# Optimization experiments

Hardware: AMD Instinct MI355X
Metric: run time of the kernel (lower is better)

The kernel has to match this reference:

```python
import jax, jax.numpy as jnp
import numpy as np

N, E, F_IN, H, C = 50000, 800000, 128, 4, 73
HC = H * C  # 292
NEG_SLOPE_ATT = 0.2   # GATv2 attention leaky relu
NEG_SLOPE_ACT = 0.01  # F.leaky_relu default
BN_EPS = 1e-5


def setup_inputs() -> dict:
    key = jax.random.key(0)
    ks = jax.random.split(key, 20)
    rn = lambda k, shp, s=0.05: (jax.random.normal(k, shp, jnp.float32) * s)
    inp = {
        'x': jax.random.normal(ks[0], (N, F_IN), jnp.float32),
        'edge_index': jax.random.randint(ks[1], (2, E), 0, N, jnp.int64),
        # conv1 (in=F_IN)
        'Wl1': rn(ks[2], (HC, F_IN)), 'bl1': rn(ks[3], (HC,)),
        'Wr1': rn(ks[4], (HC, F_IN)), 'br1': rn(ks[5], (HC,)),
        'att1': rn(ks[6], (H, C)), 'b1': rn(ks[7], (HC,)),
        # conv2 (in=HC)
        'Wl2': rn(ks[8], (HC, HC)), 'bl2': rn(ks[9], (HC,)),
        'Wr2': rn(ks[10], (HC, HC)), 'br2': rn(ks[11], (HC,)),
        'att2': rn(ks[12], (H, C)), 'b2': rn(ks[13], (HC,)),
        # shared BatchNorm1d(HC)
        'gamma': jnp.ones((HC,), jnp.float32), 'beta': jnp.zeros((HC,), jnp.float32),
        # classifier Linear(HC, 2)
        'Wc': rn(ks[14], (2, HC)), 'bc': rn(ks[15], (2,)),
    }
    return inp


def _gatv2(x, src, dst, Wl, bl, Wr, br, att, b):
    # lin_l on source, lin_r on target (PyG GATv2Conv, share_weights=False)
    xl = (x @ Wl.T + bl).reshape(-1, H, C)  # [N,H,C]
    xr = (x @ Wr.T + br).reshape(-1, H, C)
    f = xl[src] + xr[dst]                    # [E,H,C] edge-wise gather
    s = jnp.einsum('ehc,hc->eh', jax.nn.leaky_relu(f, NEG_SLOPE_ATT), att)
    # segment softmax over incoming edges of each destination node
    m = jax.ops.segment_max(s, dst, num_segments=N)
    ex = jnp.exp(s - m[dst])
    den = jax.ops.segment_sum(ex, dst, num_segments=N)
    alpha = ex / (den[dst] + 1e-16)          # [E,H]
    out = jax.ops.segment_sum(alpha[:, :, None] * xl[src], dst, num_segments=N)
    return out.reshape(-1, HC) + b           # concat heads + bias


def _bn(x, gamma, beta):
    mu = jnp.mean(x, axis=0)
    var = jnp.mean((x - mu) ** 2, axis=0)
    return (x - mu) * jax.lax.rsqrt(var + BN_EPS) * gamma + beta


def reference(x, edge_index, Wl1, bl1, Wr1, br1, att1, b1,
              Wl2, bl2, Wr2, br2, att2, b2, gamma, beta, Wc, bc):
    src, dst = edge_index[0], edge_index[1]
    h = _gatv2(x, src, dst, Wl1, bl1, Wr1, br1, att1, b1)
    h = jax.nn.leaky_relu(_bn(h, gamma, beta), NEG_SLOPE_ACT)
    h = _gatv2(h, src, dst, Wl2, bl2, Wr2, br2, att2, b2)
    h = jax.nn.leaky_relu(_bn(h, gamma, beta), NEG_SLOPE_ACT)
    return h @ Wc.T + bc
```

## Files before the change

### kernel.cpp

```cpp
#include <hip/hip_runtime.h>

#define HCDIM 292
#define NHEAD 4
#define CDIM 73
#define SLOTS 5
#define NPERM 320
#define BN_EPS 1e-5f
#define LOG2E 1.44269504f

using u16x8 = __attribute__((ext_vector_type(8))) unsigned short;
using f32x4 = __attribute__((ext_vector_type(4))) float;
using u16x4 = __attribute__((ext_vector_type(4))) unsigned short;
using hf2   = __attribute__((ext_vector_type(2))) _Float16;
using v2h   = __attribute__((ext_vector_type(2))) __fp16;
using v8h   = __attribute__((ext_vector_type(8))) __fp16;

__device__ inline v2h pkrtz(float a, float b) {
  return __builtin_amdgcn_cvt_pkrtz(a, b);
}
__device__ inline float fdot2(hf2 a, hf2 b, float c) {
  return __builtin_amdgcn_fdot2(__builtin_bit_cast(v2h, a),
                                __builtin_bit_cast(v2h, b), c, false);
}
__device__ inline ushort f2h(float f) {
  _Float16 h = (_Float16)f;
  return __builtin_bit_cast(ushort, h);
}
__device__ inline float h2f(ushort v) {
  return (float)__builtin_bit_cast(_Float16, v);
}
__device__ inline hf2 habs2(hf2 a) {
  unsigned u = __builtin_bit_cast(unsigned, a) & 0x7fff7fffu;
  return __builtin_bit_cast(hf2, u);
}

__device__ inline int perm2feat(int p, bool& valid) {
  int h, c;
  if (p < 256) {
    h = p >> 6;
    c = ((p & 3) << 4) | ((p >> 2) & 15);
    valid = true;
  } else {
    int q = p - 256;
    h = q >> 4;
    c = 64 + (q & 15);
    valid = (q & 15) < (CDIM - 64);
  }
  return h * CDIM + c;
}

__global__ void k_wperm(const float* __restrict__ W, const float* __restrict__ b,
                        ushort* __restrict__ Wp, float* __restrict__ pb,
                        int Kin, int Kpad, int kperm) {
  int p = blockIdx.x, t = threadIdx.x;
  bool pv;
  int gn = perm2feat(p, pv);
  int gk = t;
  bool kv = t < Kin;
  if (kperm) { bool v2; gk = perm2feat(t, v2); kv = v2; }
  ushort v = 0;
  if (pv && kv) v = f2h(W[(size_t)gn * Kin + gk]);
  Wp[(size_t)p * Kpad + t] = v;
  if (t == 0) pb[p] = pv ? b[gn] : 0.f;
}

__global__ void k_vecperm(const float* __restrict__ att1, const float* __restrict__ b1,
                          const float* __restrict__ att2, const float* __restrict__ b2,
                          const float* __restrict__ gamma, const float* __restrict__ beta,
                          const float* __restrict__ Wc, float* __restrict__ o) {
  int p = threadIdx.x, w = blockIdx.x;
  bool pv;
  int gn = perm2feat(p, pv);
  const float* src;
  switch (w) {
    case 0: src = att1; break;
    case 1: src = b1; break;
    case 2: src = att2; break;
    case 3: src = b2; break;
    case 4: src = gamma; break;
    case 5: src = beta; break;
    case 6: src = Wc; break;
    default: src = Wc + HCDIM; break;
  }
  o[w * NPERM + p] = pv ? src[gn] : 0.f;
}

__global__ void k_hist(const int* __restrict__ dst, int* __restrict__ deg, int E) {
  int i = blockIdx.x * blockDim.x + threadIdx.x;
  if (i < E) atomicAdd(&deg[dst[i]], 1);
}

__global__ __launch_bounds__(256) void k_block_sum(const int* __restrict__ deg,
                                                   int* __restrict__ bsum, int n) {
  __shared__ int s[256];
  int i = blockIdx.x * 256 + threadIdx.x;
  s[threadIdx.x] = (i < n) ? deg[i] : 0;
  __syncthreads();
  for (int off = 128; off > 0; off >>= 1) {
    if (threadIdx.x < off) s[threadIdx.x] += s[threadIdx.x + off];
    __syncthreads();
  }
  if (threadIdx.x == 0) bsum[blockIdx.x] = s[0];
}

__global__ __launch_bounds__(256) void k_scan_small(const int* __restrict__ bsum,
                                                    int* __restrict__ boff, int G) {
  __shared__ int s[256];
  int t = threadIdx.x;
  int v = (t < G) ? bsum[t] : 0;
  s[t] = v;
  __syncthreads();
  for (int off = 1; off < 256; off <<= 1) {
    int tv = (t >= off) ? s[t - off] : 0;
    __syncthreads();
    s[t] += tv;
    __syncthreads();
  }
  if (t < G) boff[t] = s[t] - v;
}

__global__ __launch_bounds__(256) void k_scan_final(const int* __restrict__ deg,
                                                    const int* __restrict__ boff,
                                                    int* __restrict__ row_ptr,
                                                    int* __restrict__ cursor,
                                                    int n, int E) {
  __shared__ int s[256];
  int t = threadIdx.x;
  int i = blockIdx.x * 256 + t;
  int v = (i < n) ? deg[i] : 0;
  s[t] = v;
  __syncthreads();
  for (int off = 1; off < 256; off <<= 1) {
    int tv = (t >= off) ? s[t - off] : 0;
    __syncthreads();
    s[t] += tv;
    __syncthreads();
  }
  if (i < n) {
    int rp = boff[blockIdx.x] + s[t] - v;
    row_ptr[i] = rp;
    cursor[i] = rp;
  }
  if (i == 0) row_ptr[n] = E;
}

__global__ void k_csr_fill(const int* __restrict__ srcs, const int* __restrict__ dsts,
                           int* __restrict__ cursor, int* __restrict__ csr_src, int E) {
  int i = blockIdx.x * blockDim.x + threadIdx.x;
  if (i < E) {
    int pos = atomicAdd(&cursor[dsts[i]], 1);
    csr_src[pos] = srcs[i];
  }
}

template <bool CVT>
__device__ inline void load_af(const char* const (&Ar)[4], int koff, int quad,
                               v8h (&af)[4]) {
#pragma unroll
  for (int i = 0; i < 4; ++i) {
    if (CVT) {
      const float* p = (const float*)Ar[i] + koff + quad * 8;
      float4 f0 = *(const float4*)p;
      float4 f1 = *(const float4*)(p + 4);
      union { v2h h[4]; v8h v; } u;
      u.h[0] = pkrtz(f0.x, f0.y);
      u.h[1] = pkrtz(f0.z, f0.w);
      u.h[2] = pkrtz(f1.x, f1.y);
      u.h[3] = pkrtz(f1.z, f1.w);
      af[i] = u.v;
    } else {
      af[i] = *(const v8h*)((const ushort*)Ar[i] + koff + quad * 8);
    }
  }
}

template <int KS, bool CVT>
__global__ __launch_bounds__(256) void k_gemm_blds(
    const void* __restrict__ Av, const ushort* __restrict__ Wb,
    const float* __restrict__ pb, ushort* __restrict__ o0,
    ushort* __restrict__ o1, int M, int miters) {
  constexpr int KSTEPS = KS / 32;
  constexpr int BSTR = KS + 8;
  __shared__ ushort Bs[80 * BSTR];
  int b = blockIdx.x;
  int mlo = b & 7, ct = (b >> 3) & 7, mhi = b >> 6;
  int mc = mlo + 8 * mhi;
  ushort* out = (ct < 4) ? o0 : o1;
  const int colbase = (ct & 3) * 80;
  const int tid = threadIdx.x;
  const int wave = tid >> 6, lane = tid & 63;
  const int quad = lane >> 4, lr = lane & 15;
  const int esz = CVT ? 4 : 2;

  for (int idx = tid; idx < 80 * (KS / 8); idx += 256) {
    int r = idx / (KS / 8), c8 = idx - r * (KS / 8);
    *(u16x8*)(Bs + r * BSTR + c8 * 8) =
        *(const u16x8*)(Wb + (size_t)(ct * 80 + r) * KS + c8 * 8);
  }
  __syncthreads();

  const ushort* bp[5];
#pragma unroll
  for (int i = 0; i < 5; ++i) bp[i] = Bs + (i * 16 + lr) * BSTR;

  float4 pbv[5];
#pragma unroll
  for (int ni = 0; ni < 5; ++ni)
    pbv[ni] = *(const float4*)(pb + ct * 80 + ni * 16 + quad * 4);

  for (int it = mc; it < miters; it += 64) {
    int mbase = it * 256 + wave * 64;
    const char* Ar[4];
#pragma unroll
    for (int i = 0; i < 4; ++i) {
      int ar = mbase + i * 16 + lr;
      if (ar >= M) ar = M - 1;
      Ar[i] = (const char*)Av + (size_t)ar * KS * esz;
    }
    f32x4 acc[4][5] = {};
    v8h afb[2][4];
    load_af<CVT>(Ar, 0, quad, afb[0]);
#pragma unroll
    for (int s = 0; s < KSTEPS; ++s) {
      if (s + 1 < KSTEPS) load_af<CVT>(Ar, (s + 1) * 32, quad, afb[(s + 1) & 1]);
      v8h bf[5];
#pragma unroll
      for (int i = 0; i < 5; ++i)
        bf[i] = *(const v8h*)(bp[i] + s * 32 + quad * 8);
#pragma unroll
      for (int ni = 0; ni < 5; ++ni)
#pragma unroll
        for (int mi = 0; mi < 4; ++mi)
          acc[mi][ni] = __builtin_amdgcn_mfma_f32_16x16x32_f16(
              bf[ni], afb[s & 1][mi], acc[mi][ni], 0, 0, 0);
    }
#pragma unroll
    for (int mi = 0; mi < 4; ++mi) {
      int gm = mbase + mi * 16 + lr;
      if (gm >= M) continue;
      ushort* orow = out + (size_t)gm * NPERM + colbase + quad * 4;
#pragma unroll
      for (int ni = 0; ni < 5; ++ni) {
        union { v2h h[2]; u16x4 o; } u;
        u.h[0] = pkrtz(acc[mi][ni][0] + pbv[ni].x, acc[mi][ni][1] + pbv[ni].y);
        u.h[1] = pkrtz(acc[mi][ni][2] + pbv[ni].z, acc[mi][ni][3] + pbv[ni].w);
        *(u16x4*)(orow + ni * 16) = u.o;
      }
    }
  }
}

__global__ __launch_bounds__(256) void k_pre(const ushort* __restrict__ xl,
                                             const float* __restrict__ attp,
                                             float* __restrict__ pl, int n) {
  int wave = threadIdx.x >> 6, lane = threadIdx.x & 63;
  int d = blockIdx.x * 4 + wave;
  if (d >= n) return;
  int hgrp = lane >> 4, li = lane & 15;
  const float C = 0.4f * LOG2E;
  float4 a4 = *(const float4*)(attp + lane * 4);
  hf2 av01{(_Float16)(C * a4.x), (_Float16)(C * a4.y)};
  hf2 av23{(_Float16)(C * a4.z), (_Float16)(C * a4.w)};
  hf2 av5{(_Float16)(C * attp[256 + lane]), (_Float16)0.f};

  uint2 cc = *(const uint2*)(xl + (size_t)d * NPERM + lane * 4);
  ushort c5 = xl[(size_t)d * NPERM + 256 + lane];
  hf2 c01 = __builtin_bit_cast(hf2, cc.x);
  hf2 c23 = __builtin_bit_cast(hf2, cc.y);
  hf2 c5h{__builtin_bit_cast(_Float16, c5), (_Float16)0.f};

  float Ta = fdot2(c01, av01, fdot2(c23, av23, fdot2(c5h, av5, 0.f)));
#pragma unroll
  for (int off = 1; off < 16; off <<= 1) Ta += __shfl_xor(Ta, off, 64);
  if (li == 0) pl[d * 4 + hgrp] = 1.5f * Ta;
}

__global__ __launch_bounds__(256) void k_agg(const ushort* __restrict__ xl,
                                             const ushort* __restrict__ xr,
                                             const float* __restrict__ pl,
                                             const int* __restrict__ csr_src,
                                             const int* __restrict__ row_ptr,
                                             const float* __restrict__ attp,
                                             const float* __restrict__ bp,
                                             ushort* __restrict__ out, int n) {
  int wave = threadIdx.x >> 6, lane = threadIdx.x & 63;
  int d = blockIdx.x * 4 + wave;
  if (d >= n) return;
  int hgrp = lane >> 4;
  int start = __builtin_amdgcn_readfirstlane(row_ptr[d]);
  int end = __builtin_amdgcn_readfirstlane(row_ptr[d + 1]);

  float4 bp4 = *(const float4*)(bp + lane * 4);
  float bp5 = bp[256 + lane];

  if (start >= end) {
    union { v2h h[2]; u16x4 o; } u;
    u.h[0] = pkrtz(bp4.x, bp4.y);
    u.h[1] = pkrtz(bp4.z, bp4.w);
    *(u16x4*)(out + (size_t)d * NPERM + lane * 4) = u.o;
    out[(size_t)d * NPERM + 256 + lane] = f2h(bp5);
    return;
  }

  const float C = 0.4f * LOG2E;
  float4 at4 = *(const float4*)(attp + lane * 4);
  hf2 av01{(_Float16)(C * at4.x), (_Float16)(C * at4.y)};
  hf2 av23{(_Float16)(C * at4.z), (_Float16)(C * at4.w)};
  hf2 av5{(_Float16)(C * attp[256 + lane]), (_Float16)0.f};

  hf2 xr01, xr23, xr5;
  {
    uint2 rr = *(const uint2*)(xr + (size_t)d * NPERM + lane * 4);
    xr01 = __builtin_bit_cast(hf2, rr.x);
    xr23 = __builtin_bit_cast(hf2, rr.y);
    xr5 = hf2{__builtin_bit_cast(_Float16, xr[(size_t)d * NPERM + 256 + lane]),
              (_Float16)0.f};
  }
  float Tb = fdot2(xr01, av01, fdot2(xr23, av23, fdot2(xr5, av5, 0.f)));
  Tb += __shfl_xor(Tb, 1, 64);
  Tb += __shfl_xor(Tb, 2, 64);
  Tb += __shfl_xor(Tb, 4, 64);
  Tb += __shfl_xor(Tb, 8, 64);
  float prv = 1.5f * Tb;
  float acc[SLOTS] = {};
  float den = 0.f;
  int dg = end - start;
  int nfull = dg >> 2;
  int rem = dg & 3;

  uint2 s8[4];
  ushort s1[4];
  float sp[4];
#pragma unroll
  for (int k = 0; k < 4; ++k) {
    int e = start + k;
    if (e > end - 1) e = end - 1;
    int s = __builtin_amdgcn_readfirstlane(csr_src[e]);
    s8[k] = *(const uint2*)(xl + (size_t)s * NPERM + lane * 4);
    s1[k] = xl[(size_t)s * NPERM + 256 + lane];
    sp[k] = pl[s * 4 + hgrp];
  }

  for (int g = 0; g < nfull; ++g) {
    int ebase = start + g * 4 + 4;
    uint2 n8[4];
    ushort n1[4];
    float np[4];
#pragma unroll
    for (int k = 0; k < 4; ++k) {
      int e = ebase + k;
      if (e > end - 1) e = end - 1;
      int s = __builtin_amdgcn_readfirstlane(csr_src[e]);
      n8[k] = *(const uint2*)(xl + (size_t)s * NPERM + lane * 4);
      n1[k] = xl[(size_t)s * NPERM + 256 + lane];
      np[k] = pl[s * 4 + hgrp];
    }

    hf2 x01[4], x23[4], x5[4];
    float T[4];
#pragma unroll
    for (int k = 0; k < 4; ++k) {
      x01[k] = __builtin_bit_cast(hf2, s8[k].x);
      x23[k] = __builtin_bit_cast(hf2, s8[k].y);
      x5[k] = hf2{__builtin_bit_cast(_Float16, s1[k]), (_Float16)0.f};
      T[k] = fdot2(habs2(x01[k] + xr01), av01,
             fdot2(habs2(x23[k] + xr23), av23,
             fdot2(habs2(x5[k] + xr5), av5, 0.f)));
    }
#pragma unroll
    for (int off = 1; off <= 8; off <<= 1) {
#pragma unroll
      for (int k = 0; k < 4; ++k) T[k] += __shfl_xor(T[k], off, 64);
    }
    float w[4];
#pragma unroll
    for (int k = 0; k < 4; ++k) {
      w[k] = exp2f(fminf(T[k] + sp[k] + prv, 80.f));
      den += w[k];
    }
#pragma unroll
    for (int k = 0; k < 4; ++k) {
      acc[0] = fmaf(w[k], (float)x01[k][0], acc[0]);
      acc[1] = fmaf(w[k], (float)x01[k][1], acc[1]);
      acc[2] = fmaf(w[k], (float)x23[k][0], acc[2]);
      acc[3] = fmaf(w[k], (float)x23[k][1], acc[3]);
      acc[4] = fmaf(w[k], (float)x5[k][0], acc[4]);
    }
#pragma unroll
    for (int k = 0; k < 4; ++k) { s8[k] = n8[k]; s1[k] = n1[k]; sp[k] = np[k]; }
  }

#pragma unroll
  for (int k = 0; k < 3; ++k) {
    if (k < rem) {
      hf2 x01 = __builtin_bit_cast(hf2, s8[k].x);
      hf2 x23 = __builtin_bit_cast(hf2, s8[k].y);
      hf2 x5{__builtin_bit_cast(_Float16, s1[k]), (_Float16)0.f};
      float T = fdot2(habs2(x01 + xr01), av01,
                fdot2(habs2(x23 + xr23), av23,
                fdot2(habs2(x5 + xr5), av5, 0.f)));
      T += __shfl_xor(T, 1, 64);
      T += __shfl_xor(T, 2, 64);
      T += __shfl_xor(T, 4, 64);
      T += __shfl_xor(T, 8, 64);
      float w = exp2f(fminf(T + sp[k] + prv, 80.f));
      den += w;
      acc[0] = fmaf(w, (float)x01[0], acc[0]);
      acc[1] = fmaf(w, (float)x01[1], acc[1]);
      acc[2] = fmaf(w, (float)x23[0], acc[2]);
      acc[3] = fmaf(w, (float)x23[1], acc[3]);
      acc[4] = fmaf(w, (float)x5[0], acc[4]);
    }
  }

  float inv = 1.f / (den + 1e-16f);
  union { v2h h[2]; u16x4 o; } u;
  u.h[0] = pkrtz(fmaf(acc[0], inv, bp4.x), fmaf(acc[1], inv, bp4.y));
  u.h[1] = pkrtz(fmaf(acc[2], inv, bp4.z), fmaf(acc[3], inv, bp4.w));
  *(u16x4*)(out + (size_t)d * NPERM + lane * 4) = u.o;
  out[(size_t)d * NPERM + 256 + lane] = f2h(fmaf(acc[4], inv, bp5));
}

__global__ __launch_bounds__(320) void k_bn_reduce(const ushort* __restrict__ h,
                                                   float* __restrict__ colsum,
                                                   float* __restrict__ colsq,
                                                   int n, int rows_per_block) {
  int c = threadIdx.x;
  int r0 = blockIdx.x * rows_per_block;
  int r1 = min(r0 + rows_per_block, n);
  float s = 0.f, s2 = 0.f;
  for (int r = r0; r < r1; ++r) {
    float v = h2f(h[(size_t)r * NPERM + c]);
    s += v;
    s2 += v * v;
  }
  atomicAdd(&colsum[c], s);
  atomicAdd(&colsq[c], s2);
}

__global__ void k_bn_coef(float* __restrict__ colsum, float* __restrict__ colsq,
                          const float* __restrict__ gp, const float* __restrict__ bp,
                          float invN) {
  int c = threadIdx.x + blockIdx.x * blockDim.x;
  if (c >= NPERM) return;
  float mu = colsum[c] * invN;
  float var = colsq[c] * invN - mu * mu;
  float scale = rsqrtf(var + BN_EPS) * gp[c];
  colsum[c] = scale;
  colsq[c] = bp[c] - mu * scale;
}

__global__ void k_bn_apply_bf(const ushort* __restrict__ h,
                              const float* __restrict__ scale,
                              const float* __restrict__ shift,
                              ushort* __restrict__ outb, int total8) {
  int i = blockIdx.x * blockDim.x + threadIdx.x;
  if (i >= total8) return;
  int cg = i - (i / 40) * 40;
  u16x8 v = *(const u16x8*)(h + (size_t)i * 8);
  float f[8];
#pragma unroll
  for (int k = 0; k < 8; ++k) {
    int c = cg * 8 + k;
    float t = fmaf(h2f(v[k]), scale[c], shift[c]);
    f[k] = (t > 0.f) ? t : 0.01f * t;
  }
  union { v2h h4[4]; u16x8 o; } u;
#pragma unroll
  for (int k = 0; k < 4; ++k)
    u.h4[k] = pkrtz(f[2 * k], f[2 * k + 1]);
  *(u16x8*)(outb + (size_t)i * 8) = u.o;
}

__global__ __launch_bounds__(256) void k_bn_classifier(
    const ushort* __restrict__ h, const float* __restrict__ scale,
    const float* __restrict__ shift, const float* __restrict__ wc0,
    const float* __restrict__ wc1, const float* __restrict__ bc,
    float* __restrict__ out, int n) {
  int wave = threadIdx.x >> 6, lane = threadIdx.x & 63;
  int r = blockIdx.x * 4 + wave;
  if (r >= n) return;
  float a0 = 0.f, a1 = 0.f;
#pragma unroll
  for (int k = 0; k < SLOTS; ++k) {
    int slot = lane + 64 * k;
    float v = fmaf(h2f(h[(size_t)r * NPERM + slot]), scale[slot], shift[slot]);
    v = (v > 0.f) ? v : 0.01f * v;
    a0 = fmaf(v, wc0[slot], a0);
    a1 = fmaf(v, wc1[slot], a1);
  }
#pragma unroll
  for (int off = 32; off > 0; off >>= 1) {
    a0 += __shfl_xor(a0, off, 64);
    a1 += __shfl_xor(a1, off, 64);
  }
  if (lane == 0) {
    out[(size_t)2 * r] = a0 + bc[0];
    out[(size_t)2 * r + 1] = a1 + bc[1];
  }
}

extern "C" void kernel_launch(void* const* d_in, const int* in_sizes, int n_in,
                              void* d_out, int out_size, void* d_ws, size_t ws_size,
                              hipStream_t stream) {
  const float* x      = (const float*)d_in[0];
  const int*   eidx   = (const int*)d_in[1];
  const float* Wl1    = (const float*)d_in[2];
  const float* bl1    = (const float*)d_in[3];
  const float* Wr1    = (const float*)d_in[4];
  const float* br1    = (const float*)d_in[5];
  const float* att1   = (const float*)d_in[6];
  const float* b1     = (const float*)d_in[7];
  const float* Wl2    = (const float*)d_in[8];
  const float* bl2    = (const float*)d_in[9];
  const float* Wr2    = (const float*)d_in[10];
  const float* br2    = (const float*)d_in[11];
  const float* att2   = (const float*)d_in[12];
  const float* b2     = (const float*)d_in[13];
  const float* gamma  = (const float*)d_in[14];
  const float* beta   = (const float*)d_in[15];
  const float* Wc     = (const float*)d_in[16];
  const float* bc     = (const float*)d_in[17];
  float* out = (float*)d_out;

  const int FIN = 128;
  const int N = in_sizes[0] / FIN;
  const int E = in_sizes[1] / 2;

  const int* src = eidx;
  const int* dst = eidx + E;

  ushort* h      = (ushort*)d_ws;
  ushort* xl     = h + (size_t)N * NPERM;
  ushort* xr     = xl + (size_t)N * NPERM;
  ushort* abuf   = xr + (size_t)N * NPERM;
  ushort* wb     = abuf + (size_t)N * NPERM;
  float* pb      = (float*)(wb + (size_t)2 * NPERM * NPERM);
  float* vecp    = pb + 2 * NPERM;
  float* pl      = vecp + 8 * NPERM;
  float* colsum  = pl + (size_t)N * NHEAD;
  float* colsq   = colsum + NPERM;
  int* deg       = (int*)(colsq + NPERM);
  int* row_ptr   = deg + N;
  int* cursor    = row_ptr + N + 1;
  int* bsum      = cursor + N;
  int* boff      = bsum + 256;
  int* csr_src   = boff + 256;

  const int G = (N + 255) / 256;
  const int EB = (E + 255) / 256;
  const int AGGB = (N + 3) / 4;
  const int MITERS = (N + 255) / 256;
  const int GEMMB = 512;

  const float* att1p = vecp;
  const float* b1p   = vecp + NPERM;
  const float* att2p = vecp + 2 * NPERM;
  const float* b2p   = vecp + 3 * NPERM;
  const float* gp    = vecp + 4 * NPERM;
  const float* btp   = vecp + 5 * NPERM;
  const float* wc0   = vecp + 6 * NPERM;
  const float* wc1   = vecp + 7 * NPERM;

  hipMemsetAsync(deg, 0, (size_t)N * sizeof(int), stream);
  k_hist<<<EB, 256, 0, stream>>>(dst, deg, E);
  k_block_sum<<<G, 256, 0, stream>>>(deg, bsum, N);
  k_scan_small<<<1, 256, 0, stream>>>(bsum, boff, G);
  k_scan_final<<<G, 256, 0, stream>>>(deg, boff, row_ptr, cursor, N, E);
  k_csr_fill<<<EB, 256, 0, stream>>>(src, dst, cursor, csr_src, E);

  k_vecperm<<<8, NPERM, 0, stream>>>(att1, b1, att2, b2, gamma, beta, Wc, vecp);

  k_wperm<<<NPERM, FIN, 0, stream>>>(Wl1, bl1, wb, pb, FIN, FIN, 0);
  k_wperm<<<NPERM, FIN, 0, stream>>>(Wr1, br1, wb + (size_t)NPERM * FIN, pb + NPERM,
                                     FIN, FIN, 0);
  k_gemm_blds<FIN, true><<<GEMMB, 256, 0, stream>>>((const void*)x, wb, pb,
                                                    xl, xr, N, MITERS);
  k_pre<<<AGGB, 256, 0, stream>>>(xl, att1p, pl, N);
  k_agg<<<AGGB, 256, 0, stream>>>(xl, xr, pl, csr_src, row_ptr, att1p, b1p, h, N);

  const int RPB = (N + 255) / 256;
  hipMemsetAsync(colsum, 0, 2 * NPERM * sizeof(float), stream);
  k_bn_reduce<<<256, NPERM, 0, stream>>>(h, colsum, colsq, N, RPB);
  k_bn_coef<<<2, 160, 0, stream>>>(colsum, colsq, gp, btp, 1.f / (float)N);
  k_bn_apply_bf<<<(N * 40 + 255) / 256, 256, 0, stream>>>(h, colsum, colsq, abuf,
                                                          N * 40);

  k_wperm<<<NPERM, NPERM, 0, stream>>>(Wl2, bl2, wb, pb, HCDIM, NPERM, 1);
  k_wperm<<<NPERM, NPERM, 0, stream>>>(Wr2, br2, wb + (size_t)NPERM * NPERM,
                                       pb + NPERM, HCDIM, NPERM, 1);
  k_gemm_blds<NPERM, false><<<GEMMB, 256, 0, stream>>>((const void*)abuf, wb, pb,
                                                       xl, xr, N, MITERS);
  k_pre<<<AGGB, 256, 0, stream>>>(xl, att2p, pl, N);
  k_agg<<<AGGB, 256, 0, stream>>>(xl, xr, pl, csr_src, row_ptr, att2p, b2p, h, N);

  hipMemsetAsync(colsum, 0, 2 * NPERM * sizeof(float), stream);
  k_bn_reduce<<<256, NPERM, 0, stream>>>(h, colsum, colsq, N, RPB);
  k_bn_coef<<<2, 160, 0, stream>>>(colsum, colsq, gp, btp, 1.f / (float)N);

  k_bn_classifier<<<AGGB, 256, 0, stream>>>(h, colsum, colsq, wc0, wc1, bc, out, N);
}
```

Before: 629.5 us.

## Stage A tile in LDS, fuse BN+LeakyReLU into second GEMM, merge weight perms

The GEMM now loads a 64-row A tile into LDS once, converting or normalising it on the way in. Each block covers 64 rows, with y selecting the l or r weights. Every wave takes an 80-column slice and reads B directly from global memory instead of staging B in LDS. The separate BN-apply kernel and its intermediate buffer write are removed by folding scale, shift and leaky ReLU into the second GEMM's A load. The two weight-permutation launches per layer are merged into one. The trade-off is that B is now read from global and L2 by every block rather than reused from LDS across many M iterations.

```diff
diff --git a/kernel.cpp b/kernel.cpp
--- a/kernel.cpp
+++ b/kernel.cpp
@@ -49,9 +49,14 @@
   return h * CDIM + c;
 }
 
-__global__ void k_wperm(const float* __restrict__ W, const float* __restrict__ b,
-                        ushort* __restrict__ Wp, float* __restrict__ pb,
-                        int Kin, int Kpad, int kperm) {
+__global__ void k_wperm2(const float* __restrict__ W0, const float* __restrict__ b0,
+                         const float* __restrict__ W1, const float* __restrict__ b1,
+                         ushort* __restrict__ Wp, float* __restrict__ pb,
+                         int Kin, int Kpad, int kperm) {
+  const float* W = blockIdx.y ? W1 : W0;
+  const float* b = blockIdx.y ? b1 : b0;
+  ushort* Wpo = Wp + (size_t)blockIdx.y * NPERM * Kpad;
+  float* pbo = pb + blockIdx.y * NPERM;
   int p = blockIdx.x, t = threadIdx.x;
   bool pv;
   int gn = perm2feat(p, pv);
@@ -60,8 +65,8 @@
   if (kperm) { bool v2; gk = perm2feat(t, v2); kv = v2; }
   ushort v = 0;
   if (pv && kv) v = f2h(W[(size_t)gn * Kin + gk]);
-  Wp[(size_t)p * Kpad + t] = v;
-  if (t == 0) pb[p] = pv ? b[gn] : 0.f;
+  Wpo[(size_t)p * Kpad + t] = v;
+  if (t == 0) pbo[p] = pv ? b[gn] : 0.f;
 }
 
 __global__ void k_vecperm(const float* __restrict__ att1, const float* __restrict__ b1,
@@ -153,99 +158,118 @@
   }
 }
 
-template <bool CVT>
-__device__ inline void load_af(const char* const (&Ar)[4], int koff, int quad,
-                               v8h (&af)[4]) {
-#pragma unroll
-  for (int i = 0; i < 4; ++i) {
-    if (CVT) {
-      const float* p = (const float*)Ar[i] + koff + quad * 8;
-      float4 f0 = *(const float4*)p;
-      float4 f1 = *(const float4*)(p + 4);
-      union { v2h h[4]; v8h v; } u;
-      u.h[0] = pkrtz(f0.x, f0.y);
-      u.h[1] = pkrtz(f0.z, f0.w);
-      u.h[2] = pkrtz(f1.x, f1.y);
-      u.h[3] = pkrtz(f1.z, f1.w);
-      af[i] = u.v;
-    } else {
-      af[i] = *(const v8h*)((const ushort*)Ar[i] + koff + quad * 8);
-    }
-  }
-}
-
-template <int KS, bool CVT>
-__global__ __launch_bounds__(256) void k_gemm_blds(
+template <int KS, int MODE>
+__global__ __launch_bounds__(256, 2) void k_gemm_a_lds(
     const void* __restrict__ Av, const ushort* __restrict__ Wb,
-    const float* __restrict__ pb, ushort* __restrict__ o0,
-    ushort* __restrict__ o1, int M, int miters) {
+    const float* __restrict__ pb, const float* __restrict__ bnscale,
+    const float* __restrict__ bnshift, ushort* __restrict__ o0,
+    ushort* __restrict__ o1, int M) {
   constexpr int KSTEPS = KS / 32;
-  constexpr int BSTR = KS + 8;
-  __shared__ ushort Bs[80 * BSTR];
-  int b = blockIdx.x;
-  int mlo = b & 7, ct = (b >> 3) & 7, mhi = b >> 6;
-  int mc = mlo + 8 * mhi;
-  ushort* out = (ct < 4) ? o0 : o1;
-  const int colbase = (ct & 3) * 80;
+  constexpr int STR = KS + 8;
+  __shared__ ushort As[64 * STR];
   const int tid = threadIdx.x;
+  const int rbase = blockIdx.x * 64;
+  const int y = blockIdx.y;
   const int wave = tid >> 6, lane = tid & 63;
   const int quad = lane >> 4, lr = lane & 15;
-  const int esz = CVT ? 4 : 2;
-
-  for (int idx = tid; idx < 80 * (KS / 8); idx += 256) {
-    int r = idx / (KS / 8), c8 = idx - r * (KS / 8);
-    *(u16x8*)(Bs + r * BSTR + c8 * 8) =
-        *(const u16x8*)(Wb + (size_t)(ct * 80 + r) * KS + c8 * 8);
+  const int ct = wave;
+
+  if constexpr (MODE == 0) {
+    const float* X = (const float*)Av;
+    constexpr int NIT = (64 * KS / 16) / 256;
+#pragma unroll
+    for (int k = 0; k < NIT; ++k) {
+      int idx = tid + k * 256;
+      int row = idx >> 3, sg = idx & 7;
+      int gr = rbase + row;
+      if (gr >= M) gr = M - 1;
+      const float4* p = (const float4*)(X + (size_t)gr * KS + sg * 16);
+      float4 f0 = p[0], f1 = p[1], f2 = p[2], f3 = p[3];
+      union { v2h h[4]; u16x8 v; } a, b;
+      a.h[0] = pkrtz(f0.x, f0.y); a.h[1] = pkrtz(f0.z, f0.w);
+      a.h[2] = pkrtz(f1.x, f1.y); a.h[3] = pkrtz(f1.z, f1.w);
+      b.h[0] = pkrtz(f2.x, f2.y); b.h[1] = pkrtz(f2.z, f2.w);
+      b.h[2] = pkrtz(f3.x, f3.y); b.h[3] = pkrtz(f3.z, f3.w);
+      *(u16x8*)(As + row * STR + sg * 16) = a.v;
+      *(u16x8*)(As + row * STR + sg * 16 + 8) = b.v;
+    }
+  } else {
+    const ushort* Hn = (const ushort*)Av;
+    constexpr int NIT = (64 * KS / 8) / 256;
+#pragma unroll
+    for (int k = 0; k < NIT; ++k) {
+      int idx = tid + k * 256;
+      int row = idx / (KS / 8), c8 = idx - row * (KS / 8);
+      int gr = rbase + row;
+      if (gr >= M) gr = M - 1;
+      u16x8 v = *(const u16x8*)(Hn + (size_t)gr * KS + c8 * 8);
+      int c = c8 * 8;
+      float4 s0 = *(const float4*)(bnscale + c);
+      float4 s1 = *(const float4*)(bnscale + c + 4);
+      float4 t0 = *(const float4*)(bnshift + c);
+      float4 t1 = *(const float4*)(bnshift + c + 4);
+      float f[8];
+      f[0] = fmaf(h2f(v[0]), s0.x, t0.x);
+      f[1] = fmaf(h2f(v[1]), s0.y, t0.y);
+      f[2] = fmaf(h2f(v[2]), s0.z, t0.z);
+      f[3] = fmaf(h2f(v[3]), s0.w, t0.w);
+      f[4] = fmaf(h2f(v[4]), s1.x, t1.x);
+      f[5] = fmaf(h2f(v[5]), s1.y, t1.y);
+      f[6] = fmaf(h2f(v[6]), s1.z, t1.z);
+      f[7] = fmaf(h2f(v[7]), s1.w, t1.w);
+#pragma unroll
+      for (int j = 0; j < 8; ++j) f[j] = (f[j] > 0.f) ? f[j] : 0.01f * f[j];
+      union { v2h h4[4]; u16x8 o; } u;
+#pragma unroll
+      for (int j = 0; j < 4; ++j) u.h4[j] = pkrtz(f[2 * j], f[2 * j + 1]);
+      *(u16x8*)(As + row * STR + c8 * 8) = u.o;
+    }
   }
   __syncthreads();
 
-  const ushort* bp[5];
-#pragma unroll
-  for (int i = 0; i < 5; ++i) bp[i] = Bs + (i * 16 + lr) * BSTR;
-
+  const ushort* bcol[5];
+#pragma unroll
+  for (int i = 0; i < 5; ++i)
+    bcol[i] = Wb + (size_t)(y * 320 + ct * 80 + i * 16 + lr) * KS;
+  const ushort* arow[4];
+#pragma unroll
+  for (int i = 0; i < 4; ++i) arow[i] = As + (i * 16 + lr) * STR;
+
+  f32x4 acc[4][5] = {};
+#pragma unroll
+  for (int s = 0; s < KSTEPS; ++s) {
+    v8h bf[5], af[4];
+#pragma unroll
+    for (int i = 0; i < 5; ++i)
+      bf[i] = *(const v8h*)(bcol[i] + s * 32 + quad * 8);
+#pragma unroll
+    for (int i = 0; i < 4; ++i)
+      af[i] = *(const v8h*)(arow[i] + s * 32 + quad * 8);
+#pragma unroll
+    for (int ni = 0; ni < 5; ++ni)
+#pragma unroll
+      for (int mi = 0; mi < 4; ++mi)
+        acc[mi][ni] = __builtin_amdgcn_mfma_f32_16x16x32_f16(
+            bf[ni], af[mi], acc[mi][ni], 0, 0, 0);
+  }
+
+  ushort* out = y ? o1 : o0;
+  const int colbase = ct * 80;
   float4 pbv[5];
 #pragma unroll
   for (int ni = 0; ni < 5; ++ni)
-    pbv[ni] = *(const float4*)(pb + ct * 80 + ni * 16 + quad * 4);
-
-  for (int it = mc; it < miters; it += 64) {
-    int mbase = it * 256 + wave * 64;
-    const char* Ar[4];
-#pragma unroll
-    for (int i = 0; i < 4; ++i) {
-      int ar = mbase + i * 16 + lr;
-      if (ar >= M) ar = M - 1;
-      Ar[i] = (const char*)Av + (size_t)ar * KS * esz;
-    }
-    f32x4 acc[4][5] = {};
-    v8h afb[2][4];
-    load_af<CVT>(Ar, 0, quad, afb[0]);
-#pragma unroll
-    for (int s = 0; s < KSTEPS; ++s) {
-      if (s + 1 < KSTEPS) load_af<CVT>(Ar, (s + 1) * 32, quad, afb[(s + 1) & 1]);
-      v8h bf[5];
-#pragma unroll
-      for (int i = 0; i < 5; ++i)
-        bf[i] = *(const v8h*)(bp[i] + s * 32 + quad * 8);
-#pragma unroll
-      for (int ni = 0; ni < 5; ++ni)
-#pragma unroll
-        for (int mi = 0; mi < 4; ++mi)
-          acc[mi][ni] = __builtin_amdgcn_mfma_f32_16x16x32_f16(
-              bf[ni], afb[s & 1][mi], acc[mi][ni], 0, 0, 0);
-    }
-#pragma unroll
-    for (int mi = 0; mi < 4; ++mi) {
-      int gm = mbase + mi * 16 + lr;
-      if (gm >= M) continue;
-      ushort* orow = out + (size_t)gm * NPERM + colbase + quad * 4;
-#pragma unroll
-      for (int ni = 0; ni < 5; ++ni) {
-        union { v2h h[2]; u16x4 o; } u;
-        u.h[0] = pkrtz(acc[mi][ni][0] + pbv[ni].x, acc[mi][ni][1] + pbv[ni].y);
-        u.h[1] = pkrtz(acc[mi][ni][2] + pbv[ni].z, acc[mi][ni][3] + pbv[ni].w);
-        *(u16x4*)(orow + ni * 16) = u.o;
-      }
+    pbv[ni] = *(const float4*)(pb + y * 320 + ct * 80 + ni * 16 + quad * 4);
+#pragma unroll
+  for (int mi = 0; mi < 4; ++mi) {
+    int gm = rbase + mi * 16 + lr;
+    if (gm >= M) continue;
+    ushort* orow = out + (size_t)gm * NPERM + colbase + quad * 4;
+#pragma unroll
+    for (int ni = 0; ni < 5; ++ni) {
+      union { v2h h[2]; u16x4 o; } u;
+      u.h[0] = pkrtz(acc[mi][ni][0] + pbv[ni].x, acc[mi][ni][1] + pbv[ni].y);
+      u.h[1] = pkrtz(acc[mi][ni][2] + pbv[ni].z, acc[mi][ni][3] + pbv[ni].w);
+      *(u16x4*)(orow + ni * 16) = u.o;
     }
   }
 }
@@ -448,28 +472,6 @@
   float scale = rsqrtf(var + BN_EPS) * gp[c];
   colsum[c] = scale;
   colsq[c] = bp[c] - mu * scale;
-}
-
-__global__ void k_bn_apply_bf(const ushort* __restrict__ h,
-                              const float* __restrict__ scale,
-                              const float* __restrict__ shift,
-                              ushort* __restrict__ outb, int total8) {
-  int i = blockIdx.x * blockDim.x + threadIdx.x;
-  if (i >= total8) return;
-  int cg = i - (i / 40) * 40;
-  u16x8 v = *(const u16x8*)(h + (size_t)i * 8);
-  float f[8];
-#pragma unroll
-  for (int k = 0; k < 8; ++k) {
-    int c = cg * 8 + k;
-    float t = fmaf(h2f(v[k]), scale[c], shift[c]);
-    f[k] = (t > 0.f) ? t : 0.01f * t;
-  }
-  union { v2h h4[4]; u16x8 o; } u;
-#pragma unroll
-  for (int k = 0; k < 4; ++k)
-    u.h4[k] = pkrtz(f[2 * k], f[2 * k + 1]);
-  *(u16x8*)(outb + (size_t)i * 8) = u.o;
 }
 
 __global__ __launch_bounds__(256) void k_bn_classifier(
@@ -550,8 +552,7 @@
   const int G = (N + 255) / 256;
   const int EB = (E + 255) / 256;
   const int AGGB = (N + 3) / 4;
-  const int MITERS = (N + 255) / 256;
-  const int GEMMB = 512;
+  const dim3 GEMMG((N + 63) / 64, 2);
 
   const float* att1p = vecp;
   const float* b1p   = vecp + NPERM;
@@ -571,11 +572,10 @@
 
   k_vecperm<<<8, NPERM, 0, stream>>>(att1, b1, att2, b2, gamma, beta, Wc, vecp);
 
-  k_wperm<<<NPERM, FIN, 0, stream>>>(Wl1, bl1, wb, pb, FIN, FIN, 0);
-  k_wperm<<<NPERM, FIN, 0, stream>>>(Wr1, br1, wb + (size_t)NPERM * FIN, pb + NPERM,
-                                     FIN, FIN, 0);
-  k_gemm_blds<FIN, true><<<GEMMB, 256, 0, stream>>>((const void*)x, wb, pb,
-                                                    xl, xr, N, MITERS);
+  k_wperm2<<<dim3(NPERM, 2), FIN, 0, stream>>>(Wl1, bl1, Wr1, br1, wb, pb,
+                                               FIN, FIN, 0);
+  k_gemm_a_lds<128, 0><<<GEMMG, 256, 0, stream>>>((const void*)x, wb, pb,
+                                                  nullptr, nullptr, xl, xr, N);
   k_pre<<<AGGB, 256, 0, stream>>>(xl, att1p, pl, N);
   k_agg<<<AGGB, 256, 0, stream>>>(xl, xr, pl, csr_src, row_ptr, att1p, b1p, h, N);
 
@@ -583,14 +583,11 @@
   hipMemsetAsync(colsum, 0, 2 * NPERM * sizeof(float), stream);
   k_bn_reduce<<<256, NPERM, 0, stream>>>(h, colsum, colsq, N, RPB);
   k_bn_coef<<<2, 160, 0, stream>>>(colsum, colsq, gp, btp, 1.f / (float)N);
-  k_bn_apply_bf<<<(N * 40 + 255) / 256, 256, 0, stream>>>(h, colsum, colsq, abuf,
-                                                          N * 40);
-
-  k_wperm<<<NPERM, NPERM, 0, stream>>>(Wl2, bl2, wb, pb, HCDIM, NPERM, 1);
-  k_wperm<<<NPERM, NPERM, 0, stream>>>(Wr2, br2, wb + (size_t)NPERM * NPERM,
-                                       pb + NPERM, HCDIM, NPERM, 1);
-  k_gemm_blds<NPERM, false><<<GEMMB, 256, 0, stream>>>((const void*)abuf, wb, pb,
-                                                       xl, xr, N, MITERS);
+
+  k_wperm2<<<dim3(NPERM, 2), NPERM, 0, stream>>>(Wl2, bl2, Wr2, br2, wb, pb,
+                                                 HCDIM, NPERM, 1);
+  k_gemm_a_lds<NPERM, 1><<<GEMMG, 256, 0, stream>>>((const void*)h, wb, pb,
+                                                    colsum, colsq, xl, xr, N);
   k_pre<<<AGGB, 256, 0, stream>>>(xl, att2p, pl, N);
   k_agg<<<AGGB, 256, 0, stream>>>(xl, xr, pl, csr_src, row_ptr, att2p, b2p, h, N);
 
```

Result: faster. 608.7 us (-3.3%).
